# Performance work log

Measured on AMD Instinct MI355X. Metric: run time of the kernel, lower is better.

## Reference

```python
import jax, jax.numpy as jnp
import numpy as np

B = 65536      # batch
HID = 128      # hidden_dim
Q = 4          # IRK stages
DT = 0.1       # default time step
N_ITERS = 10   # fixed-point iterations


def setup_inputs() -> dict:
    key = jax.random.key(0)
    ks = jax.random.split(key, 16)
    def lin(k, fan_in, fan_out):
        return jax.random.normal(k, (fan_in, fan_out), jnp.float32) / np.sqrt(fan_in)
    return {
        "X0": jax.random.normal(ks[0], (B, 4), jnp.float32),
        "W1": lin(ks[1], 4, HID),   "b1": jnp.zeros((HID,), jnp.float32),
        "W2": lin(ks[2], HID, HID), "b2": jnp.zeros((HID,), jnp.float32),
        "W3": lin(ks[3], HID, HID), "b3": jnp.zeros((HID,), jnp.float32),
        "W4": lin(ks[4], HID, 4),   "b4": jnp.zeros((4,), jnp.float32),
        "lam1": jax.random.normal(ks[5], (1,), jnp.float32) * 0.1 + 0.5,
        "lam2": jax.random.normal(ks[6], (1,), jnp.float32) * 0.1 + 0.5,
        "lam3": jax.random.normal(ks[7], (1,), jnp.float32) * 0.1 + 0.5,
        "lam4": jax.random.normal(ks[8], (1,), jnp.float32) * 0.1 + 0.5,
        "IRK_alpha": jax.random.normal(ks[9], (Q, Q), jnp.float32) * 0.25,
        "IRK_beta": jax.random.normal(ks[10], (Q,), jnp.float32) * 0.25,
    }


def reference(X0, W1, b1, W2, b2, W3, b3, W4, b4,
              lam1, lam2, lam3, lam4, IRK_alpha, IRK_beta):
    dt = DT

    def mlp(x):  # (N,4) -> (N,4)
        h = jnp.tanh(x @ W1 + b1)
        h = jnp.tanh(h @ W2 + b2)
        h = jnp.tanh(h @ W3 + b3)
        return h @ W4 + b4

    def hamiltonian_vf(x):  # x: (N,4) = [p1,p2,q1,q2]
        H_out = mlp(x)
        dp_dt = -lam1 * H_out[:, 2:] - lam2 * x[:, 2:]
        dq_dt = lam3 * H_out[:, :2] + lam4 * x[:, :2]
        return jnp.concatenate([dp_dt, dq_dt], axis=1)

    bsz = X0.shape[0]
    K = jnp.zeros((bsz, Q, 4), X0.dtype)
    for _ in range(N_ITERS):  # small fixed trip count, unrolled
        # same contraction as original torch einsum 'bqi,ij->bqj'
        X_stages = X0[:, None, :] + dt * jnp.einsum('bqi,ij->bqj', K, IRK_alpha)
        K = hamiltonian_vf(X_stages.reshape(-1, 4)).reshape(bsz, Q, 4)

    # intended IRK final combine: X1 = X0 + dt * sum_q beta_q K[:,q,:]
    X1 = X0 + dt * jnp.einsum('bqi,q->bi', K, IRK_beta)
    return X1
```

## Files before the change

### kernel.cpp

```cpp
#include <hip/hip_runtime.h>
#include <hip/hip_bf16.h>
#include <stdint.h>

#define HID    128
#define DT     0.1f
#define NITER  10
#define NTHR   512
#define NW     8
#define NBLK   256
#define NCH    4
#define SCALE  2.885390081777927f

typedef __attribute__((ext_vector_type(8))) short bf16x8;
typedef __attribute__((ext_vector_type(4))) float f32x4;
typedef __attribute__((ext_vector_type(4))) unsigned int u32x4;

union FragU { bf16x8 v; uint32_t u[4]; };

struct alignas(16) Smem {
    uint32_t w2f[8 * 4 * 64 * 4];
    uint32_t w3f[8 * 4 * 64 * 4];
    uint32_t w1f[8 * 64 * 4];
    uint32_t w4l[4 * 64 * 4];
    float    b1[HID], b2[HID], b3[HID];
    float    kk[NW * 32 * 4];
};

__device__ __forceinline__ uint16_t f2bf(float f) {
    uint32_t u = __float_as_uint(f);
    return (uint16_t)((u + 0x7fffu + ((u >> 16) & 1u)) >> 16);
}

__device__ __forceinline__ uint32_t pk2(float a, float b) {
    __hip_bfloat162 h = __float22bfloat162_rn(float2{a, b});
    return *reinterpret_cast<uint32_t*>(&h);
}

__device__ __forceinline__ float tanh_pre(float y) {
    float e = __builtin_amdgcn_exp2f(y);
    return fmaf(-2.0f, __builtin_amdgcn_rcpf(e + 1.0f), 1.0f);
}

__device__ __forceinline__ float uread(const float* p) {
    return __uint_as_float(__builtin_amdgcn_readfirstlane(__float_as_uint(*p)));
}

__device__ __forceinline__ bf16x8 pack2(const f32x4& a0, const f32x4& a1) {
    FragU f;
    f.u[0] = pk2(tanh_pre(a0[0]), tanh_pre(a0[1]));
    f.u[1] = pk2(tanh_pre(a0[2]), tanh_pre(a0[3]));
    f.u[2] = pk2(tanh_pre(a1[0]), tanh_pre(a1[1]));
    f.u[3] = pk2(tanh_pre(a1[2]), tanh_pre(a1[3]));
    return f.v;
}

__device__ __forceinline__ void dense_reg(
    const uint32_t* __restrict__ wf, const float* __restrict__ bias,
    bf16x8 (&bfrA)[4], bf16x8 (&bfrB)[4], int lane, int g, uint32_t zz)
{
    bf16x8 nA[4], nB[4];
    #pragma unroll
    for (int op = 0; op < 4; ++op) {
        f32x4 b0 = *(const f32x4*)&bias[(2 * op) * 16 + 4 * g + zz];
        f32x4 b1 = *(const f32x4*)&bias[(2 * op + 1) * 16 + 4 * g + zz];
        f32x4 a0A = b0, a0B = b0, a1A = b1, a1B = b1;
        __builtin_amdgcn_s_setprio(1);
        #pragma unroll
        for (int kt = 0; kt < 4; ++kt) {
            bf16x8 w0 = *(const bf16x8*)&wf[(((2 * op) * 4 + kt) * 64 + lane) * 4 + zz];
            a0A = __builtin_amdgcn_mfma_f32_16x16x32_bf16(w0, bfrA[kt], a0A, 0, 0, 0);
            a0B = __builtin_amdgcn_mfma_f32_16x16x32_bf16(w0, bfrB[kt], a0B, 0, 0, 0);
        }
        #pragma unroll
        for (int kt = 0; kt < 4; ++kt) {
            bf16x8 w1 = *(const bf16x8*)&wf[(((2 * op + 1) * 4 + kt) * 64 + lane) * 4 + zz];
            a1A = __builtin_amdgcn_mfma_f32_16x16x32_bf16(w1, bfrA[kt], a1A, 0, 0, 0);
            a1B = __builtin_amdgcn_mfma_f32_16x16x32_bf16(w1, bfrB[kt], a1B, 0, 0, 0);
        }
        __builtin_amdgcn_s_setprio(0);
        nA[op] = pack2(a0A, a1A);
        nB[op] = pack2(a0B, a1B);
    }
    #pragma unroll
    for (int kt = 0; kt < 4; ++kt) { bfrA[kt] = nA[kt]; bfrB[kt] = nB[kt]; }
}

__global__ __launch_bounds__(NTHR, 1) void pinn_irk_reg(
    const float* __restrict__ x0g,
    const float* __restrict__ w1g, const float* __restrict__ b1g,
    const float* __restrict__ w2g, const float* __restrict__ b2g,
    const float* __restrict__ w3g, const float* __restrict__ b3g,
    const float* __restrict__ w4g, const float* __restrict__ b4g,
    const float* __restrict__ l1g, const float* __restrict__ l2g,
    const float* __restrict__ l3g, const float* __restrict__ l4g,
    const float* __restrict__ alg, const float* __restrict__ beg,
    float* __restrict__ outg)
{
    __shared__ Smem S;
    const int t    = threadIdx.x;
    const int blk  = blockIdx.x;
    const int lane = t & 63;
    const int w    = t >> 6;
    const int ln   = lane & 15;
    const int g    = lane >> 4;
    const bool owner = (g == 0);

    const float L0 = uread(l1g), L1v = uread(l2g), L2v = uread(l3g), L3v = uread(l4g);
    const float B40 = uread(b4g), B41 = uread(b4g + 1);
    const float B42 = uread(b4g + 2), B43 = uread(b4g + 3);
    const float BE0 = uread(beg), BE1 = uread(beg + 1);
    const float BE2 = uread(beg + 2), BE3 = uread(beg + 3);
    float A[16];
    #pragma unroll
    for (int i = 0; i < 16; ++i) A[i] = uread(alg + i);

    for (int s = t; s < 2048; s += NTHR) {
        int lane_s = s & 63, kto = s >> 6;
        int kt = kto & 3, ot = kto >> 2;
        int m = ot * 16 + (lane_s & 15), gs = lane_s >> 4;
        uint32_t f2[4], f3[4];
        #pragma unroll
        for (int jj = 0; jj < 4; ++jj) {
            int k = 16 * (2 * kt + (jj >> 1)) + 4 * gs + 2 * (jj & 1);
            f2[jj] = (uint32_t)f2bf(w2g[k * HID + m] * SCALE)
                   | ((uint32_t)f2bf(w2g[(k + 1) * HID + m] * SCALE) << 16);
            f3[jj] = (uint32_t)f2bf(w3g[k * HID + m] * SCALE)
                   | ((uint32_t)f2bf(w3g[(k + 1) * HID + m] * SCALE) << 16);
        }
        *(u32x4*)&S.w2f[s * 4] = (u32x4){f2[0], f2[1], f2[2], f2[3]};
        *(u32x4*)&S.w3f[s * 4] = (u32x4){f3[0], f3[1], f3[2], f3[3]};
    }
    {
        int lane_s = t & 63, ot = t >> 6;
        int gs = lane_s >> 4;
        uint32_t f[4] = {0u, 0u, 0u, 0u};
        if (gs == 0) {
            int m = ot * 16 + (lane_s & 15);
            f[0] = (uint32_t)f2bf(w1g[0 * HID + m] * SCALE)
                 | ((uint32_t)f2bf(w1g[1 * HID + m] * SCALE) << 16);
            f[1] = (uint32_t)f2bf(w1g[2 * HID + m] * SCALE)
                 | ((uint32_t)f2bf(w1g[3 * HID + m] * SCALE) << 16);
        }
        *(u32x4*)&S.w1f[t * 4] = (u32x4){f[0], f[1], f[2], f[3]};
    }
    if (t < 256) {
        int lane_s = t & 63, kt = t >> 6;
        int lns = lane_s & 15, gs = lane_s >> 4;
        uint32_t f[4];
        #pragma unroll
        for (int jj = 0; jj < 4; ++jj) {
            int k0 = 16 * (2 * kt + (jj >> 1)) + 4 * gs + 2 * (jj & 1);
            uint32_t lo = (lns < 4) ? (uint32_t)f2bf(w4g[k0 * 4 + lns]) : 0u;
            uint32_t hi = (lns < 4) ? (uint32_t)f2bf(w4g[(k0 + 1) * 4 + lns]) : 0u;
            f[jj] = lo | (hi << 16);
        }
        *(u32x4*)&S.w4l[t * 4] = (u32x4){f[0], f[1], f[2], f[3]};
    }
    if (t < HID) {
        S.b1[t] = b1g[t] * SCALE;
        S.b2[t] = b2g[t] * SCALE;
        S.b3[t] = b3g[t] * SCALE;
    }
    __syncthreads();

    for (int ch = 0; ch < NCH; ++ch) {
        const int base = ((blk * NW + w) * NCH + ch) * 32;
        f32x4 XA0 = *(const f32x4*)&x0g[((base + ln) >> 2) * 4];
        f32x4 XB0 = *(const f32x4*)&x0g[((base + 16 + ln) >> 2) * 4];
        f32x4 XA = XA0, XB = XB0;
        float* kkw = &S.kk[w * 128];

        #pragma unroll 1
        for (int it = 0; it < NITER; ++it) {
            uint32_t zz = 0;
            asm volatile("" : "+v"(zz));
            zz &= ~3u;

            FragU xa, xb;
            xa.u[0] = owner ? pk2(XA[0], XA[1]) : 0u;
            xa.u[1] = owner ? pk2(XA[2], XA[3]) : 0u;
            xa.u[2] = 0u; xa.u[3] = 0u;
            xb.u[0] = owner ? pk2(XB[0], XB[1]) : 0u;
            xb.u[1] = owner ? pk2(XB[2], XB[3]) : 0u;
            xb.u[2] = 0u; xb.u[3] = 0u;

            bf16x8 bfrA[4], bfrB[4];
            #pragma unroll
            for (int op = 0; op < 4; ++op) {
                f32x4 b0 = *(const f32x4*)&S.b1[(2 * op) * 16 + 4 * g + zz];
                f32x4 b1 = *(const f32x4*)&S.b1[(2 * op + 1) * 16 + 4 * g + zz];
                bf16x8 w0 = *(const bf16x8*)&S.w1f[((2 * op) * 64 + lane) * 4 + zz];
                bf16x8 w1 = *(const bf16x8*)&S.w1f[((2 * op + 1) * 64 + lane) * 4 + zz];
                f32x4 a0A = __builtin_amdgcn_mfma_f32_16x16x32_bf16(w0, xa.v, b0, 0, 0, 0);
                f32x4 a0B = __builtin_amdgcn_mfma_f32_16x16x32_bf16(w0, xb.v, b0, 0, 0, 0);
                f32x4 a1A = __builtin_amdgcn_mfma_f32_16x16x32_bf16(w1, xa.v, b1, 0, 0, 0);
                f32x4 a1B = __builtin_amdgcn_mfma_f32_16x16x32_bf16(w1, xb.v, b1, 0, 0, 0);
                bfrA[op] = pack2(a0A, a1A);
                bfrB[op] = pack2(a0B, a1B);
            }

            dense_reg(S.w2f, S.b2, bfrA, bfrB, lane, g, zz);
            dense_reg(S.w3f, S.b3, bfrA, bfrB, lane, g, zz);

            f32x4 kA = {0.f, 0.f, 0.f, 0.f}, kB = {0.f, 0.f, 0.f, 0.f};
            __builtin_amdgcn_s_setprio(1);
            #pragma unroll
            for (int kt = 0; kt < 4; ++kt) {
                bf16x8 wfr = *(const bf16x8*)&S.w4l[(kt * 64 + lane) * 4 + zz];
                kA = __builtin_amdgcn_mfma_f32_16x16x32_bf16(wfr, bfrA[kt], kA, 0, 0, 0);
                kB = __builtin_amdgcn_mfma_f32_16x16x32_bf16(wfr, bfrB[kt], kB, 0, 0, 0);
            }
            __builtin_amdgcn_s_setprio(0);
            {
                float h0 = kA[0] + B40, h1 = kA[1] + B41;
                float h2 = kA[2] + B42, h3 = kA[3] + B43;
                f32x4 kvA = (f32x4){-L0 * h2 - L1v * XA[2], -L0 * h3 - L1v * XA[3],
                                     L2v * h0 + L3v * XA[0],  L2v * h1 + L3v * XA[1]};
                h0 = kB[0] + B40; h1 = kB[1] + B41;
                h2 = kB[2] + B42; h3 = kB[3] + B43;
                f32x4 kvB = (f32x4){-L0 * h2 - L1v * XB[2], -L0 * h3 - L1v * XB[3],
                                     L2v * h0 + L3v * XB[0],  L2v * h1 + L3v * XB[1]};
                if (owner) {
                    *(f32x4*)&kkw[ln * 4]        = kvA;
                    *(f32x4*)&kkw[(16 + ln) * 4] = kvB;
                }
                #pragma unroll
                for (int c = 0; c < 4; ++c) {
                    float sA = kvA[0] * A[c] + kvA[1] * A[4 + c]
                             + kvA[2] * A[8 + c] + kvA[3] * A[12 + c];
                    float sB = kvB[0] * A[c] + kvB[1] * A[4 + c]
                             + kvB[2] * A[8 + c] + kvB[3] * A[12 + c];
                    XA[c] = fmaf(DT, sA, XA0[c]);
                    XB[c] = fmaf(DT, sB, XB0[c]);
                }
            }
        }

        if (lane < 32) {
            int bl_ = lane >> 2, i = lane & 3;
            float s = BE0 * kkw[(bl_ * 4 + 0) * 4 + i]
                    + BE1 * kkw[(bl_ * 4 + 1) * 4 + i]
                    + BE2 * kkw[(bl_ * 4 + 2) * 4 + i]
                    + BE3 * kkw[(bl_ * 4 + 3) * 4 + i];
            int idx = base + lane;
            outg[idx] = x0g[idx] + DT * s;
        }
    }
}

extern "C" void kernel_launch(void* const* d_in, const int* in_sizes, int n_in,
                              void* d_out, int out_size, void* d_ws, size_t ws_size,
                              hipStream_t stream) {
    (void)in_sizes; (void)n_in; (void)d_ws; (void)ws_size; (void)out_size;

    dim3 grid(NBLK);
    dim3 block(NTHR);

    pinn_irk_reg<<<grid, block, 0, stream>>>(
        (const float*)d_in[0],
        (const float*)d_in[1],  (const float*)d_in[2],
        (const float*)d_in[3],  (const float*)d_in[4],
        (const float*)d_in[5],  (const float*)d_in[6],
        (const float*)d_in[7],  (const float*)d_in[8],
        (const float*)d_in[9],  (const float*)d_in[10],
        (const float*)d_in[11], (const float*)d_in[12],
        (const float*)d_in[13], (const float*)d_in[14],
        (float*)d_out);
}
```

Before: 382.3 us.

## Batch tanh reciprocals, compact W1 fragment storage, and double the grid

Replaces four per-element reciprocals in tanh with one shared reciprocal over the product of four denominators, using the batched-inverse trick, and clamps the exponent to avoid overflow. This reduces transcendental-unit pressure at the cost of extra multiplies and some precision. W1 fragments are stored compactly and zero-padded in registers, which cuts LDS footprint and read traffic. The grid doubles to 512 blocks with half the chunks per block, giving more parallelism but repeating the per-block weight setup more often.

```diff
diff --git a/kernel.cpp b/kernel.cpp
--- a/kernel.cpp
+++ b/kernel.cpp
@@ -7,12 +7,13 @@
 #define NITER  10
 #define NTHR   512
 #define NW     8
-#define NBLK   256
-#define NCH    4
+#define NBLK   512
+#define NCH    2
 #define SCALE  2.885390081777927f
 
 typedef __attribute__((ext_vector_type(8))) short bf16x8;
 typedef __attribute__((ext_vector_type(4))) float f32x4;
+typedef __attribute__((ext_vector_type(2))) unsigned int u32x2;
 typedef __attribute__((ext_vector_type(4))) unsigned int u32x4;
 
 union FragU { bf16x8 v; uint32_t u[4]; };
@@ -20,7 +21,7 @@
 struct alignas(16) Smem {
     uint32_t w2f[8 * 4 * 64 * 4];
     uint32_t w3f[8 * 4 * 64 * 4];
-    uint32_t w1f[8 * 64 * 4];
+    uint32_t w1c[8 * 16 * 2];
     uint32_t w4l[4 * 64 * 4];
     float    b1[HID], b2[HID], b3[HID];
     float    kk[NW * 32 * 4];
@@ -36,9 +37,23 @@
     return *reinterpret_cast<uint32_t*>(&h);
 }
 
-__device__ __forceinline__ float tanh_pre(float y) {
-    float e = __builtin_amdgcn_exp2f(y);
-    return fmaf(-2.0f, __builtin_amdgcn_rcpf(e + 1.0f), 1.0f);
+__device__ __forceinline__ f32x4 tanh4(f32x4 y) {
+    float e0 = __builtin_amdgcn_exp2f(fminf(y[0], 30.f)) + 1.0f;
+    float e1 = __builtin_amdgcn_exp2f(fminf(y[1], 30.f)) + 1.0f;
+    float e2 = __builtin_amdgcn_exp2f(fminf(y[2], 30.f)) + 1.0f;
+    float e3 = __builtin_amdgcn_exp2f(fminf(y[3], 30.f)) + 1.0f;
+    float p01   = e0 * e1;
+    float p012  = p01 * e2;
+    float p0123 = p012 * e3;
+    float r     = __builtin_amdgcn_rcpf(p0123);
+    float i3   = p012 * r;
+    float r012 = e3 * r;
+    float i2   = p01 * r012;
+    float r01  = e2 * r012;
+    float i1   = e0 * r01;
+    float i0   = e1 * r01;
+    return (f32x4){fmaf(-2.f, i0, 1.f), fmaf(-2.f, i1, 1.f),
+                   fmaf(-2.f, i2, 1.f), fmaf(-2.f, i3, 1.f)};
 }
 
 __device__ __forceinline__ float uread(const float* p) {
@@ -46,11 +61,13 @@
 }
 
 __device__ __forceinline__ bf16x8 pack2(const f32x4& a0, const f32x4& a1) {
+    f32x4 t0 = tanh4(a0);
+    f32x4 t1 = tanh4(a1);
     FragU f;
-    f.u[0] = pk2(tanh_pre(a0[0]), tanh_pre(a0[1]));
-    f.u[1] = pk2(tanh_pre(a0[2]), tanh_pre(a0[3]));
-    f.u[2] = pk2(tanh_pre(a1[0]), tanh_pre(a1[1]));
-    f.u[3] = pk2(tanh_pre(a1[2]), tanh_pre(a1[3]));
+    f.u[0] = pk2(t0[0], t0[1]);
+    f.u[1] = pk2(t0[2], t0[3]);
+    f.u[2] = pk2(t1[0], t1[1]);
+    f.u[3] = pk2(t1[2], t1[3]);
     return f.v;
 }
 
@@ -130,18 +147,13 @@
         *(u32x4*)&S.w2f[s * 4] = (u32x4){f2[0], f2[1], f2[2], f2[3]};
         *(u32x4*)&S.w3f[s * 4] = (u32x4){f3[0], f3[1], f3[2], f3[3]};
     }
-    {
-        int lane_s = t & 63, ot = t >> 6;
-        int gs = lane_s >> 4;
-        uint32_t f[4] = {0u, 0u, 0u, 0u};
-        if (gs == 0) {
-            int m = ot * 16 + (lane_s & 15);
-            f[0] = (uint32_t)f2bf(w1g[0 * HID + m] * SCALE)
-                 | ((uint32_t)f2bf(w1g[1 * HID + m] * SCALE) << 16);
-            f[1] = (uint32_t)f2bf(w1g[2 * HID + m] * SCALE)
-                 | ((uint32_t)f2bf(w1g[3 * HID + m] * SCALE) << 16);
-        }
-        *(u32x4*)&S.w1f[t * 4] = (u32x4){f[0], f[1], f[2], f[3]};
+    if (t < 128) {
+        int ot = t >> 4, lns = t & 15;
+        int m = ot * 16 + lns;
+        S.w1c[t * 2]     = (uint32_t)f2bf(w1g[0 * HID + m] * SCALE)
+                         | ((uint32_t)f2bf(w1g[1 * HID + m] * SCALE) << 16);
+        S.w1c[t * 2 + 1] = (uint32_t)f2bf(w1g[2 * HID + m] * SCALE)
+                         | ((uint32_t)f2bf(w1g[3 * HID + m] * SCALE) << 16);
     }
     if (t < 256) {
         int lane_s = t & 63, kt = t >> 6;
@@ -189,12 +201,17 @@
             for (int op = 0; op < 4; ++op) {
                 f32x4 b0 = *(const f32x4*)&S.b1[(2 * op) * 16 + 4 * g + zz];
                 f32x4 b1 = *(const f32x4*)&S.b1[(2 * op + 1) * 16 + 4 * g + zz];
-                bf16x8 w0 = *(const bf16x8*)&S.w1f[((2 * op) * 64 + lane) * 4 + zz];
-                bf16x8 w1 = *(const bf16x8*)&S.w1f[((2 * op + 1) * 64 + lane) * 4 + zz];
-                f32x4 a0A = __builtin_amdgcn_mfma_f32_16x16x32_bf16(w0, xa.v, b0, 0, 0, 0);
-                f32x4 a0B = __builtin_amdgcn_mfma_f32_16x16x32_bf16(w0, xb.v, b0, 0, 0, 0);
-                f32x4 a1A = __builtin_amdgcn_mfma_f32_16x16x32_bf16(w1, xa.v, b1, 0, 0, 0);
-                f32x4 a1B = __builtin_amdgcn_mfma_f32_16x16x32_bf16(w1, xb.v, b1, 0, 0, 0);
+                u32x2 c0 = *(const u32x2*)&S.w1c[((2 * op) * 16 + ln) * 2 + zz];
+                u32x2 c1 = *(const u32x2*)&S.w1c[((2 * op + 1) * 16 + ln) * 2 + zz];
+                FragU w0f, w1f;
+                w0f.u[0] = owner ? c0.x : 0u; w0f.u[1] = owner ? c0.y : 0u;
+                w0f.u[2] = 0u; w0f.u[3] = 0u;
+                w1f.u[0] = owner ? c1.x : 0u; w1f.u[1] = owner ? c1.y : 0u;
+                w1f.u[2] = 0u; w1f.u[3] = 0u;
+                f32x4 a0A = __builtin_amdgcn_mfma_f32_16x16x32_bf16(w0f.v, xa.v, b0, 0, 0, 0);
+                f32x4 a0B = __builtin_amdgcn_mfma_f32_16x16x32_bf16(w0f.v, xb.v, b0, 0, 0, 0);
+                f32x4 a1A = __builtin_amdgcn_mfma_f32_16x16x32_bf16(w1f.v, xa.v, b1, 0, 0, 0);
+                f32x4 a1B = __builtin_amdgcn_mfma_f32_16x16x32_bf16(w1f.v, xb.v, b1, 0, 0, 0);
                 bfrA[op] = pack2(a0A, a1A);
                 bfrB[op] = pack2(a0B, a1B);
             }
```

Measured after the change: 435.0 us. +13.8%, slower.
